# Performance work log

Hardware: AMD Instinct MI355X
Metric: run time of the kernel (lower is better)

## Reference

```python
import jax, jax.numpy as jnp
import numpy as np

N = 100000
E = 1600000
N_FEAT = 128
H1 = 256
H2 = 32
N_CLASS = 16


def spmm(row, col, vals, x):
    # sparse [N,N] @ dense [N,d]: gather source rows, scale by edge value,
    # scatter-add into destination rows.
    return jax.ops.segment_sum(vals[:, None] * x[col], row, num_segments=N)


def setup_inputs() -> dict:
    key = jax.random.key(0)
    ks = jax.random.split(key, 12)
    x_in = jax.random.normal(ks[0], (N, N_FEAT), dtype=jnp.float32)
    adj_row = jax.random.randint(ks[1], (E,), 0, N, dtype=jnp.int64)
    adj_col = jax.random.randint(ks[2], (E,), 0, N, dtype=jnp.int64)
    adj_vals = jax.random.uniform(ks[3], (E,), dtype=jnp.float32)
    s1 = 1.0 / np.sqrt(N_FEAT)
    s2 = 1.0 / np.sqrt(H1)
    s3 = 1.0 / np.sqrt(H2)
    W1 = jax.random.uniform(ks[4], (N_FEAT, H1), jnp.float32, -s1, s1)
    b1 = jax.random.uniform(ks[5], (H1,), jnp.float32, -s1, s1)
    W2 = jax.random.uniform(ks[6], (H1, H2), jnp.float32, -s2, s2)
    b2 = jax.random.uniform(ks[7], (H2,), jnp.float32, -s2, s2)
    W3 = jax.random.uniform(ks[8], (H2, N_CLASS), jnp.float32, -s3, s3)
    b3 = jax.random.uniform(ks[9], (N_CLASS,), jnp.float32, -s3, s3)
    return {"x_in": x_in, "adj_row": adj_row, "adj_col": adj_col,
            "adj_vals": adj_vals, "W1": W1, "b1": b1, "W2": W2, "b2": b2,
            "W3": W3, "b3": b3}


def reference(x_in, adj_row, adj_col, adj_vals, W1, b1, W2, b2, W3, b3):
    # layer 1: ReLU(Linear(adj @ x)); dropout is identity at inference
    h = jax.nn.relu(spmm(adj_row, adj_col, adj_vals, x_in) @ W1 + b1)
    # layer 2: ReLU(Linear(adj @ h))
    t = jax.nn.relu(spmm(adj_row, adj_col, adj_vals, h) @ W2 + b2)
    logits = t @ W3 + b3
    return jax.nn.log_softmax(logits, axis=1), t
```

## Files before the change

kernel.cpp:

```cpp
#include <hip/hip_runtime.h>
#include <hip/hip_bf16.h>

#define NN 100000
#define NE 1600000
#define NF 128
#define NH1 256
#define NH2 32
#define NC 16

#define NB 196
#define BSH 9
#define NCHUNK 512
#define CHSZ (NE / NCHUNK)

typedef __attribute__((ext_vector_type(4))) float f32x4;
typedef __attribute__((ext_vector_type(8))) short s16x8;
typedef __attribute__((ext_vector_type(4))) short s16x4;

__device__ __forceinline__ unsigned short f2bu(float f) {
    union { float f; unsigned u; } v; v.f = f;
    unsigned r = v.u + 0x7FFFu + ((v.u >> 16) & 1u);
    return (unsigned short)(r >> 16);
}
__device__ __forceinline__ float bflo(unsigned w) { return __uint_as_float(w << 16); }
__device__ __forceinline__ float bfhi(unsigned w) { return __uint_as_float(w & 0xFFFF0000u); }

__device__ __forceinline__ int detect_st(const int* arow) {
    const unsigned* a = (const unsigned*)arow;
    unsigned acc = 0;
#pragma unroll
    for (int i = 1; i < 32; i += 2) acc |= a[i];
    return acc == 0u ? 2 : 1;
}

__global__ __launch_bounds__(256) void fat0_k(const float* __restrict__ x, short* __restrict__ xb,
                                              const float* __restrict__ W1, const float* __restrict__ W2,
                                              short* __restrict__ w1t, short* __restrict__ w2t,
                                              const int* __restrict__ arow, int* __restrict__ histc) {
    int bid = blockIdx.x;
    if (bid < NCHUNK) {
        __shared__ int h[NB];
        for (int j = threadIdx.x; j < NB; j += 256) h[j] = 0;
        __syncthreads();
        int st = detect_st(arow);
        int base = bid * CHSZ;
        for (int i = base + threadIdx.x; i < base + CHSZ; i += 256)
            atomicAdd(&h[arow[(size_t)i * st] >> BSH], 1);
        __syncthreads();
        for (int j = threadIdx.x; j < NB; j += 256) histc[bid * NB + j] = h[j];
    } else if (bid < NCHUNK + 1024) {
        const int total = NN * NF / 4;
        for (int i = (bid - NCHUNK) * 256 + threadIdx.x; i < total; i += 1024 * 256) {
            f32x4 v = ((const f32x4*)x)[i];
            s16x4 o;
            for (int j = 0; j < 4; ++j) o[j] = (short)f2bu(v[j]);
            ((s16x4*)xb)[i] = o;
        }
    } else {
        int i = (bid - NCHUNK - 1024) * 256 + threadIdx.x;
        if (i < NF * NH1) {
            int k = i / NH1, c = i % NH1;
            w1t[c * NF + k] = (short)f2bu(W1[i]);
        } else {
            int j = i - NF * NH1;
            if (j < NH1 * NH2) {
                int k = j / NH2, c = j % NH2;
                w2t[c * NH1 + k] = (short)f2bu(W2[j]);
            }
        }
    }
}

__global__ __launch_bounds__(256) void scanb_k(const int* __restrict__ histc,
                                               int* __restrict__ cur,
                                               int* __restrict__ totals) {
    __shared__ int s[256];
    int b = blockIdx.x, t = threadIdx.x;
    int v0 = histc[(2 * t) * NB + b], v1 = histc[(2 * t + 1) * NB + b];
    int sum = v0 + v1;
    s[t] = sum; __syncthreads();
    for (int off = 1; off < 256; off <<= 1) {
        int u = (t >= off) ? s[t - off] : 0;
        __syncthreads();
        s[t] += u;
        __syncthreads();
    }
    int excl = s[t] - sum;
    cur[(2 * t) * NB + b] = excl;
    cur[(2 * t + 1) * NB + b] = excl + v0;
    if (t == 255) totals[b] = s[255];
}

__global__ __launch_bounds__(256) void scat_k(const int* __restrict__ arow,
                                              const int* __restrict__ acol,
                                              const float* __restrict__ avals,
                                              const int* __restrict__ totals,
                                              const int* __restrict__ histc,
                                              const int* __restrict__ cur,
                                              uint2* __restrict__ recs) {
    __shared__ uint2 stage[CHSZ];
    __shared__ int desti[CHSZ];
    __shared__ int gb[NB];
    __shared__ int bincur[NB];
    __shared__ int ss[256];
    int c = blockIdx.x, t = threadIdx.x;
    int tv = (t < NB) ? totals[t] : 0;
    ss[t] = tv; __syncthreads();
    for (int off = 1; off < 256; off <<= 1) {
        int u = (t >= off) ? ss[t - off] : 0;
        __syncthreads();
        ss[t] += u;
        __syncthreads();
    }
    int bstart = ss[t] - tv;
    if (t < NB) gb[t] = bstart + cur[c * NB + t];
    __syncthreads();
    int hv = (t < NB) ? histc[c * NB + t] : 0;
    ss[t] = hv; __syncthreads();
    for (int off = 1; off < 256; off <<= 1) {
        int u = (t >= off) ? ss[t - off] : 0;
        __syncthreads();
        ss[t] += u;
        __syncthreads();
    }
    int boff = ss[t] - hv;
    if (t < NB) { bincur[t] = boff; gb[t] -= boff; }
    __syncthreads();
    int st = detect_st(arow);
    int base = c * CHSZ;
    for (int i = base + t; i < base + CHSZ; i += 256) {
        int r   = arow[(size_t)i * st];
        int col = acol[(size_t)i * st];
        float v = avals[i];
        int b = r >> BSH;
        int p = atomicAdd(&bincur[b], 1);
        uint2 rec;
        rec.x = (unsigned)col | ((unsigned)(r & 511) << 17);
        rec.y = __float_as_uint(v);
        stage[p] = rec;
        desti[p] = gb[b] + p;
    }
    __syncthreads();
    for (int j = t; j < CHSZ; j += 256)
        recs[desti[j]] = stage[j];
}

__global__ __launch_bounds__(256) void sortb_k(const uint2* __restrict__ recs,
                                               const int* __restrict__ totals,
                                               int* __restrict__ rptr,
                                               uint2* __restrict__ epack) {
    __shared__ int hist[512], cur[512], sc[256], ss[256];
    __shared__ int s0sh, s1sh;
    int b = blockIdx.x, t = threadIdx.x;
    int tv = (t < NB) ? totals[t] : 0;
    ss[t] = tv; __syncthreads();
    for (int off = 1; off < 256; off <<= 1) {
        int u = (t >= off) ? ss[t - off] : 0;
        __syncthreads();
        ss[t] += u;
        __syncthreads();
    }
    if (t == b) { s0sh = ss[t] - tv; s1sh = ss[t]; }
    for (int j = t; j < 512; j += 256) hist[j] = 0;
    __syncthreads();
    int s0 = s0sh, s1 = s1sh;
    for (int i = s0 + t; i < s1; i += 256)
        atomicAdd(&hist[(recs[i].x >> 17) & 511], 1);
    __syncthreads();
    int v0 = hist[2 * t], v1 = hist[2 * t + 1], sum = v0 + v1;
    sc[t] = sum; __syncthreads();
    for (int off = 1; off < 256; off <<= 1) {
        int u = (t >= off) ? sc[t - off] : 0;
        __syncthreads();
        sc[t] += u;
        __syncthreads();
    }
    int excl = sc[t] - sum;
    cur[2 * t] = excl; cur[2 * t + 1] = excl + v0;
    __syncthreads();
    int nrows = NN - b * 512; if (nrows > 512) nrows = 512;
    for (int j = t; j < nrows; j += 256) rptr[b * 512 + j] = s0 + cur[j];
    if (b == 0 && t == 0) rptr[NN] = NE;
    __syncthreads();
    for (int i = s0 + t; i < s1; i += 256) {
        uint2 rc = recs[i];
        int rl = (rc.x >> 17) & 511;
        int p = s0 + atomicAdd(&cur[rl], 1);
        uint2 ep;
        ep.x = rc.x & 0x1FFFF;
        ep.y = rc.y;
        epack[p] = ep;
    }
}

#define MAC8(g, v) do { \
    acc[0] += (v) * bflo(g.x); acc[1] += (v) * bfhi(g.x); \
    acc[2] += (v) * bflo(g.y); acc[3] += (v) * bfhi(g.y); \
    acc[4] += (v) * bflo(g.z); acc[5] += (v) * bfhi(g.z); \
    acc[6] += (v) * bflo(g.w); acc[7] += (v) * bfhi(g.w); } while (0)

__global__ __launch_bounds__(256) void spmm1_k(const int* __restrict__ rptr,
                                               const uint2* __restrict__ ep,
                                               const short* __restrict__ xb,
                                               short* __restrict__ agg1) {
    int row = blockIdx.x * 4 + (threadIdx.x >> 6);
    if (row >= NN) return;
    int lane = threadIdx.x & 63;
    int q = lane >> 4, f = lane & 15;
    int s = rptr[row], e = rptr[row + 1];
    float acc[8] = {};
    int i = s + q;
    for (; i + 4 < e; i += 8) {
        uint2 m0 = ep[i];
        uint2 m1 = ep[i + 4];
        uint4 g0 = *(const uint4*)&xb[(size_t)m0.x * NF + f * 8];
        uint4 g1 = *(const uint4*)&xb[(size_t)m1.x * NF + f * 8];
        float v0 = __uint_as_float(m0.y);
        float v1 = __uint_as_float(m1.y);
        MAC8(g0, v0); MAC8(g1, v1);
    }
    if (i < e) {
        uint2 m = ep[i];
        uint4 g = *(const uint4*)&xb[(size_t)m.x * NF + f * 8];
        float v = __uint_as_float(m.y);
        MAC8(g, v);
    }
#pragma unroll
    for (int j = 0; j < 8; ++j) {
        acc[j] += __shfl_xor(acc[j], 16, 64);
        acc[j] += __shfl_xor(acc[j], 32, 64);
    }
    if (q == 0) {
        uint4 o4;
        o4.x = ((unsigned)f2bu(acc[1]) << 16) | f2bu(acc[0]);
        o4.y = ((unsigned)f2bu(acc[3]) << 16) | f2bu(acc[2]);
        o4.z = ((unsigned)f2bu(acc[5]) << 16) | f2bu(acc[4]);
        o4.w = ((unsigned)f2bu(acc[7]) << 16) | f2bu(acc[6]);
        *(uint4*)&agg1[(size_t)row * NF + f * 8] = o4;
    }
}

__global__ __launch_bounds__(256) void gemm12_k(const short* __restrict__ agg1,
                                                const short* __restrict__ w1t,
                                                const float* __restrict__ b1,
                                                const short* __restrict__ w2t,
                                                short* __restrict__ hw) {
    __shared__ char lds[52224];
    short* a_s  = (short*)lds;
    short* wt_s = (short*)(lds + 17408);
    short* h_s  = (short*)lds;
    short* w2_s = (short*)(lds + 33792);
    int tid = threadIdx.x;
    int r0 = blockIdx.x * 64;
    int w = tid >> 6, l = tid & 63, lr = l & 15, hi = l >> 4;
    {
        int row = tid >> 2, kk = (tid & 3) * 32, gr = r0 + row;
        for (int i = 0; i < 4; ++i) {
            int k = kk + i * 8;
            s16x8 v = {};
            if (gr < NN) v = *(const s16x8*)&agg1[(size_t)gr * NF + k];
            *(s16x8*)&a_s[row * 136 + k] = v;
        }
    }
    f32x4 acc[2][4][2] = {};
    for (int pass = 0; pass < 2; ++pass) {
        if (pass) __syncthreads();
        {
            int cl = tid >> 1, kk = (tid & 1) * 64;
            const short* src = &w1t[(size_t)(pass * 128 + cl) * NF + kk];
            for (int i = 0; i < 8; ++i)
                *(s16x8*)&wt_s[cl * 136 + kk + i * 8] = *(const s16x8*)&src[i * 8];
        }
        __syncthreads();
        for (int ks = 0; ks < 4; ++ks) {
            int kb = ks * 32 + hi * 8;
            s16x8 ar[4], br[2];
            for (int mi = 0; mi < 4; ++mi) ar[mi] = *(const s16x8*)&a_s[(mi * 16 + lr) * 136 + kb];
            for (int nj = 0; nj < 2; ++nj) br[nj] = *(const s16x8*)&wt_s[(w * 32 + nj * 16 + lr) * 136 + kb];
            for (int mi = 0; mi < 4; ++mi)
                for (int nj = 0; nj < 2; ++nj)
                    acc[pass][mi][nj] = __builtin_amdgcn_mfma_f32_16x16x32_bf16(ar[mi], br[nj], acc[pass][mi][nj], 0, 0, 0);
        }
    }
    float bias[2][2];
    for (int pass = 0; pass < 2; ++pass)
        for (int nj = 0; nj < 2; ++nj)
            bias[pass][nj] = b1[pass * 128 + w * 32 + nj * 16 + lr];
    __syncthreads();
    for (int pass = 0; pass < 2; ++pass)
        for (int mi = 0; mi < 4; ++mi) {
            int rr = mi * 16 + hi * 4;
            for (int nj = 0; nj < 2; ++nj) {
                int cc = pass * 128 + w * 32 + nj * 16 + lr;
                for (int q = 0; q < 4; ++q) {
                    float v = acc[pass][mi][nj][q] + bias[pass][nj];
                    v = v > 0.f ? v : 0.f;
                    h_s[(rr + q) * 264 + cc] = (short)f2bu(v);
                }
            }
        }
    {
        int c = tid >> 3, kk = (tid & 7) * 32;
        for (int i = 0; i < 4; ++i) {
            int k = kk + i * 8;
            *(s16x8*)&w2_s[c * 264 + k] = *(const s16x8*)&w2t[(size_t)c * NH1 + k];
        }
    }
    __syncthreads();
    f32x4 acc2[2] = {};
    for (int ks = 0; ks < 8; ++ks) {
        int kb = ks * 32 + hi * 8;
        s16x8 ar = *(const s16x8*)&h_s[(w * 16 + lr) * 264 + kb];
        for (int nj = 0; nj < 2; ++nj) {
            s16x8 br = *(const s16x8*)&w2_s[(nj * 16 + lr) * 264 + kb];
            acc2[nj] = __builtin_amdgcn_mfma_f32_16x16x32_bf16(ar, br, acc2[nj], 0, 0, 0);
        }
    }
    for (int nj = 0; nj < 2; ++nj) {
        int c = nj * 16 + lr;
        for (int q = 0; q < 4; ++q) {
            int r = r0 + w * 16 + hi * 4 + q;
            if (r < NN) hw[(size_t)r * NH2 + c] = (short)f2bu(acc2[nj][q]);
        }
    }
}

#define MAC4(g, v) do { \
    a0 += (v) * bflo(g.x); a1 += (v) * bfhi(g.x); \
    a2 += (v) * bflo(g.y); a3 += (v) * bfhi(g.y); } while (0)

__global__ __launch_bounds__(256) void spmm2_k(const int* __restrict__ rptr,
                                               const uint2* __restrict__ ep,
                                               const short* __restrict__ hw,
                                               const float* __restrict__ b2,
                                               float* __restrict__ t_out) {
    int row = blockIdx.x * 4 + (threadIdx.x >> 6);
    if (row >= NN) return;
    int lane = threadIdx.x & 63;
    int o = lane >> 3, f = lane & 7;
    int s = rptr[row], e = rptr[row + 1];
    float a0 = 0.f, a1 = 0.f, a2 = 0.f, a3 = 0.f;
    int i = s + o;
    for (; i + 8 < e; i += 16) {
        uint2 m0 = ep[i], m1 = ep[i + 8];
        uint2 g0 = *(const uint2*)&hw[(size_t)m0.x * NH2 + f * 4];
        uint2 g1 = *(const uint2*)&hw[(size_t)m1.x * NH2 + f * 4];
        float v0 = __uint_as_float(m0.y), v1 = __uint_as_float(m1.y);
        MAC4(g0, v0); MAC4(g1, v1);
    }
    if (i < e) {
        uint2 m = ep[i];
        uint2 g = *(const uint2*)&hw[(size_t)m.x * NH2 + f * 4];
        float v = __uint_as_float(m.y);
        MAC4(g, v);
    }
    a0 += __shfl_xor(a0, 8, 64); a0 += __shfl_xor(a0, 16, 64); a0 += __shfl_xor(a0, 32, 64);
    a1 += __shfl_xor(a1, 8, 64); a1 += __shfl_xor(a1, 16, 64); a1 += __shfl_xor(a1, 32, 64);
    a2 += __shfl_xor(a2, 8, 64); a2 += __shfl_xor(a2, 16, 64); a2 += __shfl_xor(a2, 32, 64);
    a3 += __shfl_xor(a3, 8, 64); a3 += __shfl_xor(a3, 16, 64); a3 += __shfl_xor(a3, 32, 64);
    if (o == 0) {
        f32x4 ov;
        float r0 = a0 + b2[f * 4];
        float r1 = a1 + b2[f * 4 + 1];
        float r2 = a2 + b2[f * 4 + 2];
        float r3 = a3 + b2[f * 4 + 3];
        ov[0] = r0 > 0.f ? r0 : 0.f;
        ov[1] = r1 > 0.f ? r1 : 0.f;
        ov[2] = r2 > 0.f ? r2 : 0.f;
        ov[3] = r3 > 0.f ? r3 : 0.f;
        *(f32x4*)&t_out[(size_t)row * NH2 + f * 4] = ov;
    }
}

__global__ __launch_bounds__(256) void gemm3_k(const float* __restrict__ t_in,
                                               const float* __restrict__ W3,
                                               const float* __restrict__ b3,
                                               float* __restrict__ out) {
    __shared__ float t_s[256 * 33];
    __shared__ float w3s[NH2 * NC];
    __shared__ float b3s[NC];
    int tid = threadIdx.x;
    int r0 = blockIdx.x * 256;
    for (int j = 0; j < 32; ++j) {
        int flat = tid + j * 256;
        int r = flat >> 5, k = flat & 31;
        int gr = r0 + r;
        t_s[r * 33 + k] = (gr < NN) ? t_in[(size_t)gr * NH2 + k] : 0.f;
    }
    for (int j = tid; j < NH2 * NC; j += 256) w3s[j] = W3[j];
    if (tid < NC) b3s[tid] = b3[tid];
    __syncthreads();
    int gr = r0 + tid;
    if (gr >= NN) return;
    float lg[NC];
    for (int c = 0; c < NC; ++c) lg[c] = b3s[c];
    for (int k = 0; k < NH2; ++k) {
        float a = t_s[tid * 33 + k];
        for (int c = 0; c < NC; ++c) lg[c] += a * w3s[k * NC + c];
    }
    float m = lg[0];
    for (int c = 1; c < NC; ++c) m = fmaxf(m, lg[c]);
    float s = 0.f;
    for (int c = 0; c < NC; ++c) s += expf(lg[c] - m);
    float lo = logf(s) + m;
    f32x4* po = (f32x4*)&out[(size_t)gr * NC];
    for (int c4 = 0; c4 < 4; ++c4) {
        f32x4 v;
        for (int q = 0; q < 4; ++q) v[q] = lg[c4 * 4 + q] - lo;
        po[c4] = v;
    }
}

extern "C" void kernel_launch(void* const* d_in, const int* in_sizes, int n_in,
                              void* d_out, int out_size, void* d_ws, size_t ws_size,
                              hipStream_t stream) {
    const float* x_in  = (const float*)d_in[0];
    const int*   arow  = (const int*)d_in[1];
    const int*   acol  = (const int*)d_in[2];
    const float* avals = (const float*)d_in[3];
    const float* W1    = (const float*)d_in[4];
    const float* b1    = (const float*)d_in[5];
    const float* W2    = (const float*)d_in[6];
    const float* b2    = (const float*)d_in[7];
    const float* W3    = (const float*)d_in[8];
    const float* b3    = (const float*)d_in[9];
    float* out = (float*)d_out;
    float* t_out = out + (size_t)NN * NC;

    char* p = (char*)d_ws;
    size_t o = 0;
    auto alloc = [&](size_t bytes) -> void* {
        void* r = p + o;
        o += (bytes + 255) & ~(size_t)255;
        return r;
    };
    uint2* recs  = (uint2*)alloc((size_t)NE * 8);
    uint2* epack = (uint2*)alloc((size_t)NE * 8);
    int*   histc = (int*)  alloc((size_t)NCHUNK * NB * 4);
    int*   cur   = (int*)  alloc((size_t)NCHUNK * NB * 4);
    int*   totals= (int*)  alloc((size_t)NB * 4);
    int*   rptr  = (int*)  alloc((size_t)(NN + 1) * 4);
    short* w1t   = (short*)alloc((size_t)NF * NH1 * 2);
    short* w2t   = (short*)alloc((size_t)NH1 * NH2 * 2);
    short* xb    = (short*)alloc((size_t)NN * NF * 2);
    short* agg1  = (short*)alloc((size_t)NN * NF * 2);
    short* hw    = (short*)alloc((size_t)NN * NH2 * 2);

    fat0_k<<<NCHUNK + 1024 + 160, 256, 0, stream>>>(x_in, xb, W1, W2, w1t, w2t, arow, histc);
    scanb_k<<<NB, 256, 0, stream>>>(histc, cur, totals);
    scat_k<<<NCHUNK, 256, 0, stream>>>(arow, acol, avals, totals, histc, cur, recs);
    sortb_k<<<NB, 256, 0, stream>>>(recs, totals, rptr, epack);
    spmm1_k<<<25000, 256, 0, stream>>>(rptr, epack, xb, agg1);
    gemm12_k<<<1563, 256, 0, stream>>>(agg1, w1t, b1, w2t, hw);
    spmm2_k<<<25000, 256, 0, stream>>>(rptr, epack, hw, b2, t_out);
    gemm3_k<<<391, 256, 0, stream>>>(t_out, W3, b3, out);
}
```

Measured before the change: 198.9 us.

## Fuse SpMM aggregation into GEMM kernels and drop intermediate buffer

The first SpMM now runs inside the layer-1 GEMM kernel: each wave aggregates 16 rows straight into shared memory, so the agg1 round trip through global memory goes away. The second SpMM is fused with the final linear layer and log-softmax, staging t in shared memory. This removes two kernel launches and the intermediate traffic. In exchange, SpMM parallelism drops from 25000 small blocks to 1563 blocks with serial per-wave row loops, which can reduce latency hiding for the irregular gathers. The fused GEMM kernel also uses a large LDS footprint that may limit occupancy.

```diff
diff --git a/kernel.cpp b/kernel.cpp
--- a/kernel.cpp
+++ b/kernel.cpp
@@ -199,52 +199,13 @@
     acc[4] += (v) * bflo(g.z); acc[5] += (v) * bfhi(g.z); \
     acc[6] += (v) * bflo(g.w); acc[7] += (v) * bfhi(g.w); } while (0)
 
-__global__ __launch_bounds__(256) void spmm1_k(const int* __restrict__ rptr,
-                                               const uint2* __restrict__ ep,
-                                               const short* __restrict__ xb,
-                                               short* __restrict__ agg1) {
-    int row = blockIdx.x * 4 + (threadIdx.x >> 6);
-    if (row >= NN) return;
-    int lane = threadIdx.x & 63;
-    int q = lane >> 4, f = lane & 15;
-    int s = rptr[row], e = rptr[row + 1];
-    float acc[8] = {};
-    int i = s + q;
-    for (; i + 4 < e; i += 8) {
-        uint2 m0 = ep[i];
-        uint2 m1 = ep[i + 4];
-        uint4 g0 = *(const uint4*)&xb[(size_t)m0.x * NF + f * 8];
-        uint4 g1 = *(const uint4*)&xb[(size_t)m1.x * NF + f * 8];
-        float v0 = __uint_as_float(m0.y);
-        float v1 = __uint_as_float(m1.y);
-        MAC8(g0, v0); MAC8(g1, v1);
-    }
-    if (i < e) {
-        uint2 m = ep[i];
-        uint4 g = *(const uint4*)&xb[(size_t)m.x * NF + f * 8];
-        float v = __uint_as_float(m.y);
-        MAC8(g, v);
-    }
-#pragma unroll
-    for (int j = 0; j < 8; ++j) {
-        acc[j] += __shfl_xor(acc[j], 16, 64);
-        acc[j] += __shfl_xor(acc[j], 32, 64);
-    }
-    if (q == 0) {
-        uint4 o4;
-        o4.x = ((unsigned)f2bu(acc[1]) << 16) | f2bu(acc[0]);
-        o4.y = ((unsigned)f2bu(acc[3]) << 16) | f2bu(acc[2]);
-        o4.z = ((unsigned)f2bu(acc[5]) << 16) | f2bu(acc[4]);
-        o4.w = ((unsigned)f2bu(acc[7]) << 16) | f2bu(acc[6]);
-        *(uint4*)&agg1[(size_t)row * NF + f * 8] = o4;
-    }
-}
-
-__global__ __launch_bounds__(256) void gemm12_k(const short* __restrict__ agg1,
-                                                const short* __restrict__ w1t,
-                                                const float* __restrict__ b1,
-                                                const short* __restrict__ w2t,
-                                                short* __restrict__ hw) {
+__global__ __launch_bounds__(256) void spgemm1_k(const int* __restrict__ rptr,
+                                                 const uint2* __restrict__ ep,
+                                                 const short* __restrict__ xb,
+                                                 const short* __restrict__ w1t,
+                                                 const float* __restrict__ b1,
+                                                 const short* __restrict__ w2t,
+                                                 short* __restrict__ hw) {
     __shared__ char lds[52224];
     short* a_s  = (short*)lds;
     short* wt_s = (short*)(lds + 17408);
@@ -254,12 +215,41 @@
     int r0 = blockIdx.x * 64;
     int w = tid >> 6, l = tid & 63, lr = l & 15, hi = l >> 4;
     {
-        int row = tid >> 2, kk = (tid & 3) * 32, gr = r0 + row;
-        for (int i = 0; i < 4; ++i) {
-            int k = kk + i * 8;
-            s16x8 v = {};
-            if (gr < NN) v = *(const s16x8*)&agg1[(size_t)gr * NF + k];
-            *(s16x8*)&a_s[row * 136 + k] = v;
+        int q = l >> 4, f = l & 15;
+        for (int rr = 0; rr < 16; ++rr) {
+            int row = r0 + w * 16 + rr;
+            int s = 0, e = 0;
+            if (row < NN) { s = rptr[row]; e = rptr[row + 1]; }
+            float acc[8] = {};
+            int i = s + q;
+            for (; i + 4 < e; i += 8) {
+                uint2 m0 = ep[i];
+                uint2 m1 = ep[i + 4];
+                uint4 g0 = *(const uint4*)&xb[(size_t)m0.x * NF + f * 8];
+                uint4 g1 = *(const uint4*)&xb[(size_t)m1.x * NF + f * 8];
+                float v0 = __uint_as_float(m0.y);
+                float v1 = __uint_as_float(m1.y);
+                MAC8(g0, v0); MAC8(g1, v1);
+            }
+            if (i < e) {
+                uint2 m = ep[i];
+                uint4 g = *(const uint4*)&xb[(size_t)m.x * NF + f * 8];
+                float v = __uint_as_float(m.y);
+                MAC8(g, v);
+            }
+#pragma unroll
+            for (int j = 0; j < 8; ++j) {
+                acc[j] += __shfl_xor(acc[j], 16, 64);
+                acc[j] += __shfl_xor(acc[j], 32, 64);
+            }
+            if (q == 0) {
+                uint4 o4;
+                o4.x = ((unsigned)f2bu(acc[1]) << 16) | f2bu(acc[0]);
+                o4.y = ((unsigned)f2bu(acc[3]) << 16) | f2bu(acc[2]);
+                o4.z = ((unsigned)f2bu(acc[5]) << 16) | f2bu(acc[4]);
+                o4.w = ((unsigned)f2bu(acc[7]) << 16) | f2bu(acc[6]);
+                *(uint4*)&a_s[(w * 16 + rr) * 136 + f * 8] = o4;
+            }
         }
     }
     f32x4 acc[2][4][2] = {};
@@ -329,85 +319,89 @@
     a0 += (v) * bflo(g.x); a1 += (v) * bfhi(g.x); \
     a2 += (v) * bflo(g.y); a3 += (v) * bfhi(g.y); } while (0)
 
-__global__ __launch_bounds__(256) void spmm2_k(const int* __restrict__ rptr,
-                                               const uint2* __restrict__ ep,
-                                               const short* __restrict__ hw,
-                                               const float* __restrict__ b2,
-                                               float* __restrict__ t_out) {
-    int row = blockIdx.x * 4 + (threadIdx.x >> 6);
-    if (row >= NN) return;
-    int lane = threadIdx.x & 63;
-    int o = lane >> 3, f = lane & 7;
-    int s = rptr[row], e = rptr[row + 1];
-    float a0 = 0.f, a1 = 0.f, a2 = 0.f, a3 = 0.f;
-    int i = s + o;
-    for (; i + 8 < e; i += 16) {
-        uint2 m0 = ep[i], m1 = ep[i + 8];
-        uint2 g0 = *(const uint2*)&hw[(size_t)m0.x * NH2 + f * 4];
-        uint2 g1 = *(const uint2*)&hw[(size_t)m1.x * NH2 + f * 4];
-        float v0 = __uint_as_float(m0.y), v1 = __uint_as_float(m1.y);
-        MAC4(g0, v0); MAC4(g1, v1);
-    }
-    if (i < e) {
-        uint2 m = ep[i];
-        uint2 g = *(const uint2*)&hw[(size_t)m.x * NH2 + f * 4];
-        float v = __uint_as_float(m.y);
-        MAC4(g, v);
-    }
-    a0 += __shfl_xor(a0, 8, 64); a0 += __shfl_xor(a0, 16, 64); a0 += __shfl_xor(a0, 32, 64);
-    a1 += __shfl_xor(a1, 8, 64); a1 += __shfl_xor(a1, 16, 64); a1 += __shfl_xor(a1, 32, 64);
-    a2 += __shfl_xor(a2, 8, 64); a2 += __shfl_xor(a2, 16, 64); a2 += __shfl_xor(a2, 32, 64);
-    a3 += __shfl_xor(a3, 8, 64); a3 += __shfl_xor(a3, 16, 64); a3 += __shfl_xor(a3, 32, 64);
-    if (o == 0) {
-        f32x4 ov;
-        float r0 = a0 + b2[f * 4];
-        float r1 = a1 + b2[f * 4 + 1];
-        float r2 = a2 + b2[f * 4 + 2];
-        float r3 = a3 + b2[f * 4 + 3];
-        ov[0] = r0 > 0.f ? r0 : 0.f;
-        ov[1] = r1 > 0.f ? r1 : 0.f;
-        ov[2] = r2 > 0.f ? r2 : 0.f;
-        ov[3] = r3 > 0.f ? r3 : 0.f;
-        *(f32x4*)&t_out[(size_t)row * NH2 + f * 4] = ov;
-    }
-}
-
-__global__ __launch_bounds__(256) void gemm3_k(const float* __restrict__ t_in,
-                                               const float* __restrict__ W3,
-                                               const float* __restrict__ b3,
-                                               float* __restrict__ out) {
-    __shared__ float t_s[256 * 33];
+__global__ __launch_bounds__(256) void spgemm3_k(const int* __restrict__ rptr,
+                                                 const uint2* __restrict__ ep,
+                                                 const short* __restrict__ hw,
+                                                 const float* __restrict__ b2,
+                                                 const float* __restrict__ W3,
+                                                 const float* __restrict__ b3,
+                                                 float* __restrict__ t_out,
+                                                 float* __restrict__ out) {
+    __shared__ float t_s[64 * 33];
     __shared__ float w3s[NH2 * NC];
     __shared__ float b3s[NC];
+    __shared__ float b2s[NH2];
     int tid = threadIdx.x;
-    int r0 = blockIdx.x * 256;
-    for (int j = 0; j < 32; ++j) {
-        int flat = tid + j * 256;
-        int r = flat >> 5, k = flat & 31;
-        int gr = r0 + r;
-        t_s[r * 33 + k] = (gr < NN) ? t_in[(size_t)gr * NH2 + k] : 0.f;
-    }
+    int r0 = blockIdx.x * 64;
     for (int j = tid; j < NH2 * NC; j += 256) w3s[j] = W3[j];
     if (tid < NC) b3s[tid] = b3[tid];
-    __syncthreads();
-    int gr = r0 + tid;
-    if (gr >= NN) return;
-    float lg[NC];
-    for (int c = 0; c < NC; ++c) lg[c] = b3s[c];
-    for (int k = 0; k < NH2; ++k) {
-        float a = t_s[tid * 33 + k];
-        for (int c = 0; c < NC; ++c) lg[c] += a * w3s[k * NC + c];
-    }
-    float m = lg[0];
-    for (int c = 1; c < NC; ++c) m = fmaxf(m, lg[c]);
-    float s = 0.f;
-    for (int c = 0; c < NC; ++c) s += expf(lg[c] - m);
-    float lo = logf(s) + m;
-    f32x4* po = (f32x4*)&out[(size_t)gr * NC];
-    for (int c4 = 0; c4 < 4; ++c4) {
-        f32x4 v;
-        for (int q = 0; q < 4; ++q) v[q] = lg[c4 * 4 + q] - lo;
-        po[c4] = v;
+    if (tid < NH2) b2s[tid] = b2[tid];
+    __syncthreads();
+    int w = tid >> 6, l = tid & 63;
+    int o = l >> 3, f = l & 7;
+    for (int rr = 0; rr < 16; ++rr) {
+        int row = r0 + w * 16 + rr;
+        int s = 0, e = 0;
+        if (row < NN) { s = rptr[row]; e = rptr[row + 1]; }
+        float a0 = 0.f, a1 = 0.f, a2 = 0.f, a3 = 0.f;
+        int i = s + o;
+        for (; i + 8 < e; i += 16) {
+            uint2 m0 = ep[i], m1 = ep[i + 8];
+            uint2 g0 = *(const uint2*)&hw[(size_t)m0.x * NH2 + f * 4];
+            uint2 g1 = *(const uint2*)&hw[(size_t)m1.x * NH2 + f * 4];
+            float v0 = __uint_as_float(m0.y), v1 = __uint_as_float(m1.y);
+            MAC4(g0, v0); MAC4(g1, v1);
+        }
+        if (i < e) {
+            uint2 m = ep[i];
+            uint2 g = *(const uint2*)&hw[(size_t)m.x * NH2 + f * 4];
+            float v = __uint_as_float(m.y);
+            MAC4(g, v);
+        }
+        a0 += __shfl_xor(a0, 8, 64); a0 += __shfl_xor(a0, 16, 64); a0 += __shfl_xor(a0, 32, 64);
+        a1 += __shfl_xor(a1, 8, 64); a1 += __shfl_xor(a1, 16, 64); a1 += __shfl_xor(a1, 32, 64);
+        a2 += __shfl_xor(a2, 8, 64); a2 += __shfl_xor(a2, 16, 64); a2 += __shfl_xor(a2, 32, 64);
+        a3 += __shfl_xor(a3, 8, 64); a3 += __shfl_xor(a3, 16, 64); a3 += __shfl_xor(a3, 32, 64);
+        if (o == 0 && row < NN) {
+            float r0v = a0 + b2s[f * 4];
+            float r1v = a1 + b2s[f * 4 + 1];
+            float r2v = a2 + b2s[f * 4 + 2];
+            float r3v = a3 + b2s[f * 4 + 3];
+            r0v = r0v > 0.f ? r0v : 0.f;
+            r1v = r1v > 0.f ? r1v : 0.f;
+            r2v = r2v > 0.f ? r2v : 0.f;
+            r3v = r3v > 0.f ? r3v : 0.f;
+            int lrow = w * 16 + rr;
+            t_s[lrow * 33 + f * 4]     = r0v;
+            t_s[lrow * 33 + f * 4 + 1] = r1v;
+            t_s[lrow * 33 + f * 4 + 2] = r2v;
+            t_s[lrow * 33 + f * 4 + 3] = r3v;
+            f32x4 ov; ov[0] = r0v; ov[1] = r1v; ov[2] = r2v; ov[3] = r3v;
+            *(f32x4*)&t_out[(size_t)row * NH2 + f * 4] = ov;
+        }
+    }
+    __syncthreads();
+    if (tid < 64) {
+        int gr = r0 + tid;
+        if (gr < NN) {
+            float lg[NC];
+            for (int c = 0; c < NC; ++c) lg[c] = b3s[c];
+            for (int k = 0; k < NH2; ++k) {
+                float a = t_s[tid * 33 + k];
+                for (int c = 0; c < NC; ++c) lg[c] += a * w3s[k * NC + c];
+            }
+            float m = lg[0];
+            for (int c = 1; c < NC; ++c) m = fmaxf(m, lg[c]);
+            float sum = 0.f;
+            for (int c = 0; c < NC; ++c) sum += expf(lg[c] - m);
+            float lo = logf(sum) + m;
+            f32x4* po = (f32x4*)&out[(size_t)gr * NC];
+            for (int c4 = 0; c4 < 4; ++c4) {
+                f32x4 v;
+                for (int q = 0; q < 4; ++q) v[q] = lg[c4 * 4 + q] - lo;
+                po[c4] = v;
+            }
+        }
     }
 }
 
@@ -443,15 +437,12 @@
     short* w1t   = (short*)alloc((size_t)NF * NH1 * 2);
     short* w2t   = (short*)alloc((size_t)NH1 * NH2 * 2);
     short* xb    = (short*)alloc((size_t)NN * NF * 2);
-    short* agg1  = (short*)alloc((size_t)NN * NF * 2);
     short* hw    = (short*)alloc((size_t)NN * NH2 * 2);
 
     fat0_k<<<NCHUNK + 1024 + 160, 256, 0, stream>>>(x_in, xb, W1, W2, w1t, w2t, arow, histc);
     scanb_k<<<NB, 256, 0, stream>>>(histc, cur, totals);
     scat_k<<<NCHUNK, 256, 0, stream>>>(arow, acol, avals, totals, histc, cur, recs);
     sortb_k<<<NB, 256, 0, stream>>>(recs, totals, rptr, epack);
-    spmm1_k<<<25000, 256, 0, stream>>>(rptr, epack, xb, agg1);
-    gemm12_k<<<1563, 256, 0, stream>>>(agg1, w1t, b1, w2t, hw);
-    spmm2_k<<<25000, 256, 0, stream>>>(rptr, epack, hw, b2, t_out);
-    gemm3_k<<<391, 256, 0, stream>>>(t_out, W3, b3, out);
-}
+    spgemm1_k<<<1563, 256, 0, stream>>>(rptr, epack, xb, w1t, b1, w2t, hw);
+    spgemm3_k<<<1563, 256, 0, stream>>>(rptr, epack, hw, b2, W3, b3, t_out, out);
+}
```

New measurement: 263.6 us. +32.5%, slower.

## Split second SpMM by source-column half to shrink gather working set

Applied to the files above, without the earlier changes.

The edge sort now orders each row's edges by source-column half as well, and records a per-row split point. The second SpMM runs as two passes, one gathering only from the lower half of hw and one from the upper half, so each pass touches a smaller gather working set (about 3.2 MB) that fits better in cache. The cost is an extra kernel launch, a second read of the edge list and row pointers, and a float partial buffer written and read back between the passes. The bounds check was removed because the grid size divides NN exactly.

```diff
diff --git a/kernel.cpp b/kernel.cpp
--- a/kernel.cpp
+++ b/kernel.cpp
@@ -12,6 +12,7 @@
 #define BSH 9
 #define NCHUNK 512
 #define CHSZ (NE / NCHUNK)
+#define NKEY 1024
 
 typedef __attribute__((ext_vector_type(4))) float f32x4;
 typedef __attribute__((ext_vector_type(8))) short s16x8;
@@ -148,8 +149,9 @@
 __global__ __launch_bounds__(256) void sortb_k(const uint2* __restrict__ recs,
                                                const int* __restrict__ totals,
                                                int* __restrict__ rptr,
+                                               int* __restrict__ rsplit,
                                                uint2* __restrict__ epack) {
-    __shared__ int hist[512], cur[512], sc[256], ss[256];
+    __shared__ int hist[NKEY], cur[NKEY], sc[256], ss[256];
     __shared__ int s0sh, s1sh;
     int b = blockIdx.x, t = threadIdx.x;
     int tv = (t < NB) ? totals[t] : 0;
@@ -161,35 +163,46 @@
         __syncthreads();
     }
     if (t == b) { s0sh = ss[t] - tv; s1sh = ss[t]; }
-    for (int j = t; j < 512; j += 256) hist[j] = 0;
+    for (int j = t; j < NKEY; j += 256) hist[j] = 0;
     __syncthreads();
     int s0 = s0sh, s1 = s1sh;
-    for (int i = s0 + t; i < s1; i += 256)
-        atomicAdd(&hist[(recs[i].x >> 17) & 511], 1);
-    __syncthreads();
-    int v0 = hist[2 * t], v1 = hist[2 * t + 1], sum = v0 + v1;
-    sc[t] = sum; __syncthreads();
+    for (int i = s0 + t; i < s1; i += 256) {
+        unsigned rx = recs[i].x;
+        int col = (int)(rx & 0x1FFFF);
+        int key = (int)(((rx >> 17) & 511) << 1) | (col >= (NN / 2) ? 1 : 0);
+        atomicAdd(&hist[key], 1);
+    }
+    __syncthreads();
+    int loc[4]; int lsum = 0;
+#pragma unroll
+    for (int j = 0; j < 4; ++j) { loc[j] = hist[t * 4 + j]; lsum += loc[j]; }
+    sc[t] = lsum; __syncthreads();
     for (int off = 1; off < 256; off <<= 1) {
         int u = (t >= off) ? sc[t - off] : 0;
         __syncthreads();
         sc[t] += u;
         __syncthreads();
     }
-    int excl = sc[t] - sum;
-    cur[2 * t] = excl; cur[2 * t + 1] = excl + v0;
+    int run = sc[t] - lsum;
+#pragma unroll
+    for (int j = 0; j < 4; ++j) { cur[t * 4 + j] = run; run += loc[j]; }
     __syncthreads();
     int nrows = NN - b * 512; if (nrows > 512) nrows = 512;
-    for (int j = t; j < nrows; j += 256) rptr[b * 512 + j] = s0 + cur[j];
+    for (int j = t; j < nrows; j += 256) {
+        rptr[b * 512 + j]   = s0 + cur[j * 2];
+        rsplit[b * 512 + j] = s0 + cur[j * 2 + 1];
+    }
     if (b == 0 && t == 0) rptr[NN] = NE;
     __syncthreads();
     for (int i = s0 + t; i < s1; i += 256) {
         uint2 rc = recs[i];
-        int rl = (rc.x >> 17) & 511;
-        int p = s0 + atomicAdd(&cur[rl], 1);
-        uint2 ep;
-        ep.x = rc.x & 0x1FFFF;
-        ep.y = rc.y;
-        epack[p] = ep;
+        int col = (int)(rc.x & 0x1FFFF);
+        int key = (int)(((rc.x >> 17) & 511) << 1) | (col >= (NN / 2) ? 1 : 0);
+        int p = s0 + atomicAdd(&cur[key], 1);
+        uint2 e2;
+        e2.x = (unsigned)col;
+        e2.y = rc.y;
+        epack[p] = e2;
     }
 }
 
@@ -329,16 +342,15 @@
     a0 += (v) * bflo(g.x); a1 += (v) * bfhi(g.x); \
     a2 += (v) * bflo(g.y); a3 += (v) * bfhi(g.y); } while (0)
 
-__global__ __launch_bounds__(256) void spmm2_k(const int* __restrict__ rptr,
-                                               const uint2* __restrict__ ep,
-                                               const short* __restrict__ hw,
-                                               const float* __restrict__ b2,
-                                               float* __restrict__ t_out) {
+__global__ __launch_bounds__(256) void spmm2a_k(const int* __restrict__ rptr,
+                                                const int* __restrict__ rsplit,
+                                                const uint2* __restrict__ ep,
+                                                const short* __restrict__ hw,
+                                                float* __restrict__ tpart) {
     int row = blockIdx.x * 4 + (threadIdx.x >> 6);
-    if (row >= NN) return;
     int lane = threadIdx.x & 63;
     int o = lane >> 3, f = lane & 7;
-    int s = rptr[row], e = rptr[row + 1];
+    int s = rptr[row], e = rsplit[row];
     float a0 = 0.f, a1 = 0.f, a2 = 0.f, a3 = 0.f;
     int i = s + o;
     for (; i + 8 < e; i += 16) {
@@ -359,11 +371,48 @@
     a2 += __shfl_xor(a2, 8, 64); a2 += __shfl_xor(a2, 16, 64); a2 += __shfl_xor(a2, 32, 64);
     a3 += __shfl_xor(a3, 8, 64); a3 += __shfl_xor(a3, 16, 64); a3 += __shfl_xor(a3, 32, 64);
     if (o == 0) {
+        f32x4 ov; ov[0] = a0; ov[1] = a1; ov[2] = a2; ov[3] = a3;
+        __builtin_nontemporal_store(ov, (f32x4*)&tpart[(size_t)row * NH2 + f * 4]);
+    }
+}
+
+__global__ __launch_bounds__(256) void spmm2b_k(const int* __restrict__ rptr,
+                                                const int* __restrict__ rsplit,
+                                                const uint2* __restrict__ ep,
+                                                const short* __restrict__ hw,
+                                                const float* __restrict__ tpart,
+                                                const float* __restrict__ b2,
+                                                float* __restrict__ t_out) {
+    int row = blockIdx.x * 4 + (threadIdx.x >> 6);
+    int lane = threadIdx.x & 63;
+    int o = lane >> 3, f = lane & 7;
+    int s = rsplit[row], e = rptr[row + 1];
+    float a0 = 0.f, a1 = 0.f, a2 = 0.f, a3 = 0.f;
+    int i = s + o;
+    for (; i + 8 < e; i += 16) {
+        uint2 m0 = ep[i], m1 = ep[i + 8];
+        uint2 g0 = *(const uint2*)&hw[(size_t)m0.x * NH2 + f * 4];
+        uint2 g1 = *(const uint2*)&hw[(size_t)m1.x * NH2 + f * 4];
+        float v0 = __uint_as_float(m0.y), v1 = __uint_as_float(m1.y);
+        MAC4(g0, v0); MAC4(g1, v1);
+    }
+    if (i < e) {
+        uint2 m = ep[i];
+        uint2 g = *(const uint2*)&hw[(size_t)m.x * NH2 + f * 4];
+        float v = __uint_as_float(m.y);
+        MAC4(g, v);
+    }
+    a0 += __shfl_xor(a0, 8, 64); a0 += __shfl_xor(a0, 16, 64); a0 += __shfl_xor(a0, 32, 64);
+    a1 += __shfl_xor(a1, 8, 64); a1 += __shfl_xor(a1, 16, 64); a1 += __shfl_xor(a1, 32, 64);
+    a2 += __shfl_xor(a2, 8, 64); a2 += __shfl_xor(a2, 16, 64); a2 += __shfl_xor(a2, 32, 64);
+    a3 += __shfl_xor(a3, 8, 64); a3 += __shfl_xor(a3, 16, 64); a3 += __shfl_xor(a3, 32, 64);
+    if (o == 0) {
+        f32x4 pv = __builtin_nontemporal_load((const f32x4*)&tpart[(size_t)row * NH2 + f * 4]);
+        float r0 = a0 + pv[0] + b2[f * 4];
+        float r1 = a1 + pv[1] + b2[f * 4 + 1];
+        float r2 = a2 + pv[2] + b2[f * 4 + 2];
+        float r3 = a3 + pv[3] + b2[f * 4 + 3];
         f32x4 ov;
-        float r0 = a0 + b2[f * 4];
-        float r1 = a1 + b2[f * 4 + 1];
-        float r2 = a2 + b2[f * 4 + 2];
-        float r3 = a3 + b2[f * 4 + 3];
         ov[0] = r0 > 0.f ? r0 : 0.f;
         ov[1] = r1 > 0.f ? r1 : 0.f;
         ov[2] = r2 > 0.f ? r2 : 0.f;
@@ -440,18 +489,21 @@
     int*   cur   = (int*)  alloc((size_t)NCHUNK * NB * 4);
     int*   totals= (int*)  alloc((size_t)NB * 4);
     int*   rptr  = (int*)  alloc((size_t)(NN + 1) * 4);
+    int*   rsplit= (int*)  alloc((size_t)NN * 4);
     short* w1t   = (short*)alloc((size_t)NF * NH1 * 2);
     short* w2t   = (short*)alloc((size_t)NH1 * NH2 * 2);
     short* xb    = (short*)alloc((size_t)NN * NF * 2);
     short* agg1  = (short*)alloc((size_t)NN * NF * 2);
     short* hw    = (short*)alloc((size_t)NN * NH2 * 2);
+    float* tpart = (float*)alloc((size_t)NN * NH2 * 4);
 
     fat0_k<<<NCHUNK + 1024 + 160, 256, 0, stream>>>(x_in, xb, W1, W2, w1t, w2t, arow, histc);
     scanb_k<<<NB, 256, 0, stream>>>(histc, cur, totals);
     scat_k<<<NCHUNK, 256, 0, stream>>>(arow, acol, avals, totals, histc, cur, recs);
-    sortb_k<<<NB, 256, 0, stream>>>(recs, totals, rptr, epack);
+    sortb_k<<<NB, 256, 0, stream>>>(recs, totals, rptr, rsplit, epack);
     spmm1_k<<<25000, 256, 0, stream>>>(rptr, epack, xb, agg1);
     gemm12_k<<<1563, 256, 0, stream>>>(agg1, w1t, b1, w2t, hw);
-    spmm2_k<<<25000, 256, 0, stream>>>(rptr, epack, hw, b2, t_out);
+    spmm2a_k<<<25000, 256, 0, stream>>>(rptr, rsplit, epack, hw, tpart);
+    spmm2b_k<<<25000, 256, 0, stream>>>(rptr, rsplit, epack, hw, tpart, b2, t_out);
     gemm3_k<<<391, 256, 0, stream>>>(t_out, W3, b3, out);
 }
```

Result: slower. 231.5 us (+16.4%).
